# Kernel optimization log

Measured on AMD Instinct MI355X. Metric: run time of the kernel, lower is better.

Reference implementation:

```python
import jax, jax.numpy as jnp
import numpy as np

EPS = 1e-6   # torch F.pairwise_distance default eps
BIG = 1e30   # stand-in for +inf on invalid DP cells (fp32-safe)


def _pairwise_dist(observed, modeled):
    # dist[b, i, j] = || observed[b, i, :] - modeled[b, j, :] + eps ||_2
    diff = observed[:, :, None, :] - modeled[:, None, :, :] + EPS  # [B,T,T,D]
    return jnp.sqrt(jnp.sum(diff * diff, axis=-1))                 # [B,T,T]


def _dtw(dist):
    # Anti-diagonal (wavefront) DTW: diagonal k holds cells (i, j=k-i).
    B, T, _ = dist.shape
    dist_flat = dist.reshape(B, T * T)
    ii = jnp.arange(T)

    d0 = jnp.full((B, T), BIG, dist.dtype).at[:, 0].set(dist[:, 0, 0])
    dm1 = jnp.full((B, T), BIG, dist.dtype)
    pad = jnp.full((B, 1), BIG, dist.dtype)

    def step(carry, k):
        prev2, prev = carry                      # diagonals k-2, k-1, each [B,T] indexed by i
        jj = k - ii
        valid = (jj >= 0) & (jj < T)
        lin = ii * T + jnp.clip(jj, 0, T - 1)
        dd = jnp.take(dist_flat, lin, axis=1)    # dist along diagonal k, [B,T]
        sh_prev = jnp.concatenate([pad, prev[:, :-1]], axis=1)    # dtw[i-1, j]
        sh_prev2 = jnp.concatenate([pad, prev2[:, :-1]], axis=1)  # dtw[i-1, j-1]
        best = jnp.minimum(jnp.minimum(sh_prev, prev), sh_prev2)  # prev = dtw[i, j-1]
        cur = jnp.where(valid[None, :], dd + best, BIG)
        return (prev, cur), None

    (_, last), _ = jax.lax.scan(step, (dm1, d0), jnp.arange(1, 2 * T - 1))
    return last[:, T - 1]  # dtw[T-1, T-1] per batch element


def setup_inputs() -> dict:
    key = jax.random.key(0)
    k1, k2 = jax.random.split(key)
    B, T, D = 8, 1024, 8
    observed = jax.random.normal(k1, (B, T, D), dtype=jnp.float32)
    modeled = jax.random.normal(k2, (B, T, D), dtype=jnp.float32)
    return {"observed": observed, "modeled": modeled}


def reference(observed, modeled):
    dist = _pairwise_dist(observed, modeled)   # [B,T,T]
    dtw_distance = _dtw(dist)                  # [B]
    return jnp.mean(dtw_distance)
```

## Files before the change

kernel.cpp:

```cpp
#include <hip/hip_runtime.h>

#define T_LEN  1024
#define D_DIM  8
#define BIGV   1e30f
#define EPSV   1e-6f
#define RB     256
#define NTILE  17
#define TSTEPS 1088
#define NSLOT  16
#define NW3    8
#define NSS3   32

typedef _Float16 half2v __attribute__((ext_vector_type(2)));
typedef unsigned u32x4  __attribute__((ext_vector_type(4)));

__device__ __forceinline__ float dpp_shr1(float x) {
  int xi = __builtin_bit_cast(int, x);
  int r = __builtin_amdgcn_update_dpp(xi, xi, 0x138, 0xf, 0xf, false);
  return __builtin_bit_cast(float, r);
}
__device__ __forceinline__ float dpp_shl1(float x) {
  int xi = __builtin_bit_cast(int, x);
  int r = __builtin_amdgcn_update_dpp(xi, xi, 0x130, 0xf, 0xf, false);
  return __builtin_bit_cast(float, r);
}

#define GLOADO(dst, addr, OFF)                                             \
  asm volatile("global_load_dwordx4 %0, %1, off offset:" #OFF             \
               : "=v"(dst) : "v"(addr))

__global__ __launch_bounds__(256)
void dist4_kernel(const float* __restrict__ obs, const float* __restrict__ mod,
                  _Float16* __restrict__ dist) {
  const int q  = threadIdx.x & 63;
  const int wv = threadIdx.x >> 6;
  const int lt = blockIdx.x % NTILE;
  const int lg = blockIdx.x / NTILE;
  const int l  = lg * 4 + wv;
  const int s  = blockIdx.y;
  const int b  = blockIdx.z;
  const int t  = lt * 64 + q;
  const int cloc = t - l;
  const int row  = (s < 8) ? (64 * s + l) : (1023 - (64 * (s - 8) + l));

  float dd = __builtin_inff();
  if ((unsigned)cloc < (unsigned)T_LEN) {
    const int cg = (s < 8) ? cloc : (1023 - cloc);
    const float4* o4 = (const float4*)(obs + ((size_t)b * T_LEN + row) * D_DIM);
    const float4* m4 = (const float4*)(mod + ((size_t)b * T_LEN + cg) * D_DIM);
    float4 a0 = o4[0], a1 = o4[1], c0 = m4[0], c1 = m4[1];
    float acc = 0.f, df;
    df = a0.x - c0.x + EPSV; acc = fmaf(df, df, acc);
    df = a0.y - c0.y + EPSV; acc = fmaf(df, df, acc);
    df = a0.z - c0.z + EPSV; acc = fmaf(df, df, acc);
    df = a0.w - c0.w + EPSV; acc = fmaf(df, df, acc);
    df = a1.x - c1.x + EPSV; acc = fmaf(df, df, acc);
    df = a1.y - c1.y + EPSV; acc = fmaf(df, df, acc);
    df = a1.z - c1.z + EPSV; acc = fmaf(df, df, acc);
    df = a1.w - c1.w + EPSV; acc = fmaf(df, df, acc);
    dd = sqrtf(acc);
  }
  dist[(((size_t)(b * NSLOT + s) * NTILE + lt) * 64 + l) * 64 + q] = (_Float16)dd;
}

#define DTW_STEPX(DD, Q)                                                   \
  {                                                                        \
    const float dd_ = (DD);                                                \
    float cu = dpp_shr1(c);                                                \
    cu = lane0 ? rv : cu;                                                  \
    float best = fminf(fminf(cu, cuPrev), c);                              \
    if ((Q) == 0 && LT == 0) { if (w0 && lane0) best = 0.f; }              \
    float cv = dd_ + best;                                                 \
    cuPrev = cu;                                                           \
    c = cv;                                                                \
    rv = dpp_shl1(rv);                                                     \
    out = dpp_shl1(out);                                                   \
    out = lane63 ? c : out;                                                \
  }

#define DTW_STEP2X(U, QB)                                                  \
  {                                                                        \
    half2v hh_ = __builtin_bit_cast(half2v, (unsigned)(U));                \
    DTW_STEPX((float)hh_[0], (QB))                                         \
    DTW_STEPX((float)hh_[1], (QB) + 1)                                     \
  }

#define DTW_STEP8X(V, QB)                                                  \
  DTW_STEP2X((V)[0], (QB))                                                 \
  DTW_STEP2X((V)[1], (QB) + 2)                                             \
  DTW_STEP2X((V)[2], (QB) + 4)                                             \
  DTW_STEP2X((V)[3], (QB) + 6)

#define DTW_TILEX(SS, C0, C1, C2, C3, C4, C5, C6, C7,                      \
                      N0, N1, N2, N3, N4, N5, N6, N7)                      \
  {                                                                        \
    const int T0 = ((SS) - 2 * w) * 64;                                    \
    if (T0 >= 0 && T0 < TSTEPS) {                                          \
      const int LT = T0 >> 6;                                              \
      if (LT < NTILE - 1) {                                                \
        const void* np_ = (const void*)(base + (size_t)(LT + 1) * 4096);   \
        GLOADO(N0, np_, 0);   GLOADO(N1, np_, 16);                         \
        GLOADO(N2, np_, 32);  GLOADO(N3, np_, 48);                         \
        GLOADO(N4, np_, 64);  GLOADO(N5, np_, 80);                         \
        GLOADO(N6, np_, 96);  GLOADO(N7, np_, 112);                        \
        asm volatile("s_waitcnt vmcnt(8)" ::: "memory");                   \
      } else {                                                             \
        asm volatile("s_waitcnt vmcnt(0)" ::: "memory");                   \
      }                                                                    \
      __builtin_amdgcn_sched_barrier(0);                                   \
      float rv;                                                            \
      if (w0) { rv = BIGV; }                                               \
      else    { rv = ringbuf[w - 1][(T0 + l) & (RB - 1)]; }                \
      float out = 0.f;                                                     \
      DTW_STEP8X(C0, 0)  DTW_STEP8X(C1, 8)  DTW_STEP8X(C2, 16)             \
      DTW_STEP8X(C3, 24) DTW_STEP8X(C4, 32) DTW_STEP8X(C5, 40)             \
      DTW_STEP8X(C6, 48) DTW_STEP8X(C7, 56)                                \
      const int e_ = T0 - 63 + l;                                          \
      if ((unsigned)e_ < (unsigned)T_LEN) {                                \
        if (wlast) rowg[e_] = out;                                         \
        else       ringbuf[w][e_ & (RB - 1)] = out;                        \
      }                                                                    \
    }                                                                      \
  }

__global__ __launch_bounds__(512)
void dtw11_kernel(const _Float16* __restrict__ dist, float* __restrict__ rows) {
  __shared__ float ringbuf[NW3 - 1][RB];

  const int tid  = threadIdx.x;
  const int half = blockIdx.x;
  const int b    = blockIdx.y;
  const int l    = tid & 63;
  const int w    = tid >> 6;
  const bool lane0  = (l == 0);
  const bool lane63 = (l == 63);
  const bool w0     = (w == 0);
  const bool wlast  = (w == NW3 - 1);
  const int  s      = half * 8 + w;

  float* rowg = rows + ((size_t)b * 2 + half) * T_LEN;

  {
    float* rp = &ringbuf[0][0];
    for (int k = tid; k < (NW3 - 1) * RB; k += 512) rp[k] = BIGV;
  }

  const _Float16* base = dist + (size_t)(b * NSLOT + s) * NTILE * 4096 + l * 64;

  u32x4 a0, a1, a2, a3, a4, a5, a6, a7;
  u32x4 b0, b1, b2, b3, b4, b5, b6, b7;
  {
    const void* tp = (const void*)base;
    GLOADO(a0, tp, 0);   GLOADO(a1, tp, 16);
    GLOADO(a2, tp, 32);  GLOADO(a3, tp, 48);
    GLOADO(a4, tp, 64);  GLOADO(a5, tp, 80);
    GLOADO(a6, tp, 96);  GLOADO(a7, tp, 112);
    asm volatile("s_waitcnt vmcnt(0)" ::: "memory");
    __builtin_amdgcn_sched_barrier(0);
  }
  b0 = a0; b1 = a1; b2 = a2; b3 = a3; b4 = a4; b5 = a5; b6 = a6; b7 = a7;

  __syncthreads();

  float c = BIGV, cuPrev = BIGV;

  for (int ss = 0; ss < NSS3; ss += 2) {
    DTW_TILEX(ss,     a0, a1, a2, a3, a4, a5, a6, a7,
                      b0, b1, b2, b3, b4, b5, b6, b7)
    __syncthreads();
    DTW_TILEX(ss + 1, b0, b1, b2, b3, b4, b5, b6, b7,
                      a0, a1, a2, a3, a4, a5, a6, a7)
    __syncthreads();
  }
}

__global__ __launch_bounds__(1024)
void combine_kernel(const float* __restrict__ rows, float* __restrict__ bres) {
  __shared__ unsigned gmin;
  const int b = blockIdx.x;
  const int tid = threadIdx.x;
  if (tid == 0) gmin = 0x7f800000u;
  __syncthreads();
  const float* rowf = rows + (size_t)b * 2 * T_LEN;
  const float* rowb = rowf + T_LEN;
  const int j = tid;
  float b1v = rowb[1023 - j];
  float b2v = (j < 1023) ? rowb[1022 - j] : BIGV;
  float v = rowf[j] + fminf(b1v, b2v);
  for (int m = 1; m < 64; m <<= 1) v = fminf(v, __shfl_xor(v, m, 64));
  if ((tid & 63) == 0) atomicMin(&gmin, __float_as_uint(v));
  __syncthreads();
  if (tid == 0) bres[b] = __uint_as_float(gmin);
}

#define NWAVE  16
#define NSS    47
__global__ __launch_bounds__(1024)
void dtw_fused_kernel(const float* __restrict__ obs, const float* __restrict__ mod,
                      float* __restrict__ bres) {
  __shared__ float ringbuf[NWAVE - 1][RB];
  __shared__ float modl[T_LEN * D_DIM];

  const int tid = threadIdx.x;
  const int b   = blockIdx.x;
  const int l   = tid & 63;
  const int w   = tid >> 6;

  const float4* msrc = (const float4*)(mod + (size_t)b * T_LEN * D_DIM);
  float4* mdst = (float4*)modl;
  mdst[tid]        = msrc[tid];
  mdst[tid + 1024] = msrc[tid + 1024];
  const float* orow = obs + ((size_t)b * T_LEN + w * 64 + l) * D_DIM;
  float4 a0 = ((const float4*)orow)[0];
  float4 a1 = ((const float4*)orow)[1];
  float obsp[8] = {a0.x + EPSV, a0.y + EPSV, a0.z + EPSV, a0.w + EPSV,
                   a1.x + EPSV, a1.y + EPSV, a1.z + EPSV, a1.w + EPSV};
  float mrow[8] = {0.f, 0.f, 0.f, 0.f, 0.f, 0.f, 0.f, 0.f};
  __syncthreads();

  float c = BIGV, p = BIGV, rprev = BIGV;
  const bool lane0  = (l == 0);
  const bool lane63 = (l == 63);
  const int  rdw    = (w > 0) ? (w - 1) : 0;
  const bool w0     = (w == 0);
  const bool wlast  = (w == NWAVE - 1);

  for (int ss = 0; ss < NSS; ++ss) {
    const int t0 = (ss - 2 * w) * 64;
    if (t0 >= 0 && t0 < TSTEPS) {
#pragma unroll 8
      for (int q = 0; q < 64; ++q) {
        const int t = t0 + q;
#pragma unroll
        for (int d = 0; d < 8; ++d) mrow[d] = dpp_shr1(mrow[d]);
        if (lane0) {
          const int tm = (t < T_LEN) ? t : (T_LEN - 1);
          const float4* mr = (const float4*)(modl + tm * 8);
          float4 m0 = mr[0], m1 = mr[1];
          mrow[0] = m0.x; mrow[1] = m0.y; mrow[2] = m0.z; mrow[3] = m0.w;
          mrow[4] = m1.x; mrow[5] = m1.y; mrow[6] = m1.z; mrow[7] = m1.w;
        }
        float acc = 0.f;
#pragma unroll
        for (int d = 0; d < 8; ++d) { float df = obsp[d] - mrow[d]; acc = fmaf(df, df, acc); }
        float dd = sqrtf(acc);

        float c_up = dpp_shr1(c);
        float p_up = dpp_shr1(p);
        float ringv = ringbuf[rdw][t & (RB - 1)];
        if (lane0) { c_up = w0 ? BIGV : ringv; p_up = w0 ? BIGV : rprev; }
        rprev = ringv;

        const int j = t - l;
        const bool valid = ((unsigned)j < (unsigned)T_LEN);
        float best = fminf(fminf(c_up, p_up), c);
        if (w0 && t == 0) { if (lane0) best = 0.f; }
        float cur = valid ? (dd + best) : BIGV;
        p = c; c = cur;

        if (lane63 && !wlast && t >= 63 && t < TSTEPS - 1)
          ringbuf[w][(t - 63) & (RB - 1)] = c;
      }
    }
    __syncthreads();
  }
  if (tid == 1023) bres[b] = p;
}

__global__ void mean_kernel(const float* __restrict__ bres, float* __restrict__ out, int B) {
  if (threadIdx.x == 0) {
    float s = 0.f;
    for (int i = 0; i < B; ++i) s += bres[i];
    out[0] = s / (float)B;
  }
}

extern "C" void kernel_launch(void* const* d_in, const int* in_sizes, int n_in,
                              void* d_out, int out_size, void* d_ws, size_t ws_size,
                              hipStream_t stream) {
  (void)n_in; (void)out_size;
  const float* obs = (const float*)d_in[0];
  const float* mod = (const float*)d_in[1];
  float* out = (float*)d_out;
  const int B = in_sizes[0] / (T_LEN * D_DIM);

  float* bres = (float*)d_ws;
  float* rows = (float*)((char*)d_ws + 256);
  _Float16* dist = (_Float16*)((char*)d_ws + 256 + (size_t)B * 2 * T_LEN * 4);
  const size_t need = 256 + (size_t)B * 2 * T_LEN * 4
                    + (size_t)B * NSLOT * NTILE * 4096 * sizeof(_Float16);

  if (ws_size >= need) {
    dist4_kernel<<<dim3(NTILE * 16, NSLOT, B), 256, 0, stream>>>(obs, mod, dist);
    dtw11_kernel<<<dim3(2, B), 512, 0, stream>>>(dist, rows);
    combine_kernel<<<B, 1024, 0, stream>>>(rows, bres);
  } else {
    dtw_fused_kernel<<<B, 1024, 0, stream>>>(obs, mod, bres);
  }
  mean_kernel<<<1, 64, 0, stream>>>(bres, out, B);
}
```

Measured before the change: 89.50 us.

## Process two DTW rows per lane with four-wave wavefront over packed fp16 pairs

Adds a new dist6/dtw13 path in which each lane handles two consecutive DTW rows, so a half-problem is covered by 4 waves of 128 rows each instead of 8 waves of 64. The distance kernel packs the two rows' fp16 distances into one 32-bit word to match this layout. The aim is to cut the number of inter-wave pipeline stages and barriers on the serial wavefront critical path. In exchange each step does twice the work per lane, there are more tile steps per wave, and more registers are used for the double-buffered tiles. The old path remains as a fallback when the workspace is too small.

```diff
diff --git a/kernel.cpp b/kernel.cpp
--- a/kernel.cpp
+++ b/kernel.cpp
@@ -5,6 +5,12 @@
 #define BIGV   1e30f
 #define EPSV   1e-6f
 #define RB     256
+
+#define NT2   18
+#define TS2   1152
+#define NW1   4
+#define NSS1  28
+
 #define NTILE  17
 #define TSTEPS 1088
 #define NSLOT  16
@@ -28,6 +34,215 @@
 #define GLOADO(dst, addr, OFF)                                             \
   asm volatile("global_load_dwordx4 %0, %1, off offset:" #OFF             \
                : "=v"(dst) : "v"(addr))
+
+
+__global__ __launch_bounds__(256)
+void dist6_kernel(const float* __restrict__ obs, const float* __restrict__ mod,
+                  unsigned* __restrict__ dist) {
+  const int q  = threadIdx.x & 63;
+  const int wv = threadIdx.x >> 6;
+  const int lt = blockIdx.x % NT2;
+  const int lg = blockIdx.x / NT2;
+  const int l  = lg * 4 + wv;
+  const int s  = blockIdx.y;
+  const int h  = s >> 2;
+  const int w  = s & 3;
+  const int b  = blockIdx.z;
+  const int t  = lt * 64 + q;
+  const int R0 = 128 * w + 2 * l;
+  const int colA = t - 2 * l;
+  const int colB = colA - 1;
+
+  float vA = __builtin_inff(), vB = __builtin_inff();
+  if ((unsigned)colA < (unsigned)T_LEN) {
+    const int rg = h ? (1023 - R0) : R0;
+    const int cg = h ? (1023 - colA) : colA;
+    const float4* o4 = (const float4*)(obs + ((size_t)b * T_LEN + rg) * D_DIM);
+    const float4* m4 = (const float4*)(mod + ((size_t)b * T_LEN + cg) * D_DIM);
+    float4 a0 = o4[0], a1 = o4[1], c0 = m4[0], c1 = m4[1];
+    float acc = 0.f, df;
+    df = a0.x - c0.x + EPSV; acc = fmaf(df, df, acc);
+    df = a0.y - c0.y + EPSV; acc = fmaf(df, df, acc);
+    df = a0.z - c0.z + EPSV; acc = fmaf(df, df, acc);
+    df = a0.w - c0.w + EPSV; acc = fmaf(df, df, acc);
+    df = a1.x - c1.x + EPSV; acc = fmaf(df, df, acc);
+    df = a1.y - c1.y + EPSV; acc = fmaf(df, df, acc);
+    df = a1.z - c1.z + EPSV; acc = fmaf(df, df, acc);
+    df = a1.w - c1.w + EPSV; acc = fmaf(df, df, acc);
+    vA = sqrtf(acc);
+  }
+  if ((unsigned)colB < (unsigned)T_LEN) {
+    const int rg = h ? (1023 - (R0 + 1)) : (R0 + 1);
+    const int cg = h ? (1023 - colB) : colB;
+    const float4* o4 = (const float4*)(obs + ((size_t)b * T_LEN + rg) * D_DIM);
+    const float4* m4 = (const float4*)(mod + ((size_t)b * T_LEN + cg) * D_DIM);
+    float4 a0 = o4[0], a1 = o4[1], c0 = m4[0], c1 = m4[1];
+    float acc = 0.f, df;
+    df = a0.x - c0.x + EPSV; acc = fmaf(df, df, acc);
+    df = a0.y - c0.y + EPSV; acc = fmaf(df, df, acc);
+    df = a0.z - c0.z + EPSV; acc = fmaf(df, df, acc);
+    df = a0.w - c0.w + EPSV; acc = fmaf(df, df, acc);
+    df = a1.x - c1.x + EPSV; acc = fmaf(df, df, acc);
+    df = a1.y - c1.y + EPSV; acc = fmaf(df, df, acc);
+    df = a1.z - c1.z + EPSV; acc = fmaf(df, df, acc);
+    df = a1.w - c1.w + EPSV; acc = fmaf(df, df, acc);
+    vB = sqrtf(acc);
+  }
+  const unsigned hA = __builtin_bit_cast(unsigned short, (_Float16)vA);
+  const unsigned hB = __builtin_bit_cast(unsigned short, (_Float16)vB);
+  dist[(((size_t)(b * 8 + s) * NT2 + lt) * 64 + l) * 64 + q] = (hB << 16) | hA;
+}
+
+#define DTW_STEPQ2(U, QQ)                                                  \
+  {                                                                        \
+    half2v hh_ = __builtin_bit_cast(half2v, (unsigned)(U));                \
+    const float ddA_ = (float)hh_[0];                                      \
+    const float ddB_ = (float)hh_[1];                                      \
+    float bU  = dpp_shr1(bC);                                              \
+    float bU2 = dpp_shr1(bP);                                              \
+    bU  = lane0 ? rv  : bU;                                                \
+    bU2 = lane0 ? rvo : bU2;                                               \
+    float bestA = fminf(fminf(bU, bU2), aC);                               \
+    if ((QQ) == 0 && LT == 0) { if (w0 && lane0) bestA = 0.f; }            \
+    const float newA = ddA_ + bestA;                                       \
+    const float bestB = fminf(fminf(aC, aP), bC);                          \
+    const float newB = ddB_ + bestB;                                       \
+    aP = aC; aC = newA; bP = bC; bC = newB;                                \
+    rvo = rv; rv = dpp_shl1(rv);                                           \
+    out = dpp_shl1(out);                                                   \
+    out = lane63 ? bC : out;                                               \
+  }
+
+#define DTW_STEP42(V, QB)                                                  \
+  DTW_STEPQ2((V)[0], (QB))                                                 \
+  DTW_STEPQ2((V)[1], (QB) + 1)                                             \
+  DTW_STEPQ2((V)[2], (QB) + 2)                                             \
+  DTW_STEPQ2((V)[3], (QB) + 3)
+
+#define DTW_TILE13(SS, C0,C1,C2,C3,C4,C5,C6,C7,C8,C9,C10,C11,C12,C13,C14,C15, \
+                       N0,N1,N2,N3,N4,N5,N6,N7,N8,N9,N10,N11,N12,N13,N14,N15) \
+  {                                                                        \
+    const int T0 = ((SS) - 3 * w) * 64;                                    \
+    if (T0 >= 0 && T0 < TS2) {                                             \
+      const int LT = T0 >> 6;                                              \
+      if (LT < NT2 - 1) {                                                  \
+        const void* np_ = (const void*)(base + (size_t)(LT + 1) * 4096);   \
+        GLOADO(N0,  np_, 0);    GLOADO(N1,  np_, 16);                      \
+        GLOADO(N2,  np_, 32);   GLOADO(N3,  np_, 48);                      \
+        GLOADO(N4,  np_, 64);   GLOADO(N5,  np_, 80);                      \
+        GLOADO(N6,  np_, 96);   GLOADO(N7,  np_, 112);                     \
+        GLOADO(N8,  np_, 128);  GLOADO(N9,  np_, 144);                     \
+        GLOADO(N10, np_, 160);  GLOADO(N11, np_, 176);                     \
+        GLOADO(N12, np_, 192);  GLOADO(N13, np_, 208);                     \
+        GLOADO(N14, np_, 224);  GLOADO(N15, np_, 240);                     \
+        asm volatile("s_waitcnt vmcnt(16)" ::: "memory");                  \
+      } else {                                                             \
+        asm volatile("s_waitcnt vmcnt(0)" ::: "memory");                   \
+      }                                                                    \
+      __builtin_amdgcn_sched_barrier(0);                                   \
+      float rv, rvo;                                                       \
+      if (w0) { rv = BIGV; rvo = BIGV; }                                   \
+      else {                                                               \
+        rv  = ringbuf[w - 1][(T0 + l) & (RB - 1)];                         \
+        rvo = (LT == 0) ? BIGV : ringbuf[w - 1][(T0 - 1) & (RB - 1)];      \
+      }                                                                    \
+      float out = 0.f;                                                     \
+      DTW_STEP42(C0, 0)   DTW_STEP42(C1, 4)   DTW_STEP42(C2, 8)            \
+      DTW_STEP42(C3, 12)  DTW_STEP42(C4, 16)  DTW_STEP42(C5, 20)           \
+      DTW_STEP42(C6, 24)  DTW_STEP42(C7, 28)  DTW_STEP42(C8, 32)           \
+      DTW_STEP42(C9, 36)  DTW_STEP42(C10, 40) DTW_STEP42(C11, 44)          \
+      DTW_STEP42(C12, 48) DTW_STEP42(C13, 52) DTW_STEP42(C14, 56)          \
+      DTW_STEP42(C15, 60)                                                  \
+      const int e_ = T0 - 127 + l;                                         \
+      if ((unsigned)e_ < (unsigned)T_LEN) {                                \
+        if (wlast) rowg[e_] = out;                                         \
+        else       ringbuf[w][e_ & (RB - 1)] = out;                        \
+      }                                                                    \
+    }                                                                      \
+  }
+
+__global__ __launch_bounds__(256)
+void dtw13_kernel(const unsigned* __restrict__ dist, float* __restrict__ rows) {
+  __shared__ float ringbuf[NW1 - 1][RB];
+
+  const int tid  = threadIdx.x;
+  const int h    = blockIdx.x;
+  const int b    = blockIdx.y;
+  const int l    = tid & 63;
+  const int w    = tid >> 6;
+  const bool lane0  = (l == 0);
+  const bool lane63 = (l == 63);
+  const bool w0     = (w == 0);
+  const bool wlast  = (w == NW1 - 1);
+
+  float* rowg = rows + ((size_t)b * 2 + h) * T_LEN;
+
+  {
+    float* rp = &ringbuf[0][0];
+    for (int k = tid; k < (NW1 - 1) * RB; k += 256) rp[k] = BIGV;
+  }
+
+  const unsigned* base = dist + (size_t)(b * 8 + h * 4 + w) * NT2 * 4096 + l * 64;
+
+  u32x4 a0,a1,a2,a3,a4,a5,a6,a7,a8,a9,a10,a11,a12,a13,a14,a15;
+  u32x4 b0,b1,b2,b3,b4,b5,b6,b7,b8,b9,b10,b11,b12,b13,b14,b15;
+  {
+    const void* tp = (const void*)base;
+    GLOADO(a0,  tp, 0);    GLOADO(a1,  tp, 16);
+    GLOADO(a2,  tp, 32);   GLOADO(a3,  tp, 48);
+    GLOADO(a4,  tp, 64);   GLOADO(a5,  tp, 80);
+    GLOADO(a6,  tp, 96);   GLOADO(a7,  tp, 112);
+    GLOADO(a8,  tp, 128);  GLOADO(a9,  tp, 144);
+    GLOADO(a10, tp, 160);  GLOADO(a11, tp, 176);
+    GLOADO(a12, tp, 192);  GLOADO(a13, tp, 208);
+    GLOADO(a14, tp, 224);  GLOADO(a15, tp, 240);
+    asm volatile("s_waitcnt vmcnt(0)" ::: "memory");
+    __builtin_amdgcn_sched_barrier(0);
+  }
+  b0=a0; b1=a1; b2=a2; b3=a3; b4=a4; b5=a5; b6=a6; b7=a7;
+  b8=a8; b9=a9; b10=a10; b11=a11; b12=a12; b13=a13; b14=a14; b15=a15;
+
+  __syncthreads();
+
+  float aC = BIGV, aP = BIGV, bC = BIGV, bP = BIGV;
+
+  for (int ss = 0; ss < NSS1; ss += 2) {
+    DTW_TILE13(ss,     a0,a1,a2,a3,a4,a5,a6,a7,a8,a9,a10,a11,a12,a13,a14,a15,
+                       b0,b1,b2,b3,b4,b5,b6,b7,b8,b9,b10,b11,b12,b13,b14,b15)
+    __syncthreads();
+    DTW_TILE13(ss + 1, b0,b1,b2,b3,b4,b5,b6,b7,b8,b9,b10,b11,b12,b13,b14,b15,
+                       a0,a1,a2,a3,a4,a5,a6,a7,a8,a9,a10,a11,a12,a13,a14,a15)
+    __syncthreads();
+  }
+  (void)aP; (void)bP;
+}
+
+__global__ __launch_bounds__(1024)
+void combine_kernel(const float* __restrict__ rows, float* __restrict__ bres) {
+  __shared__ unsigned gmin;
+  const int b = blockIdx.x;
+  const int tid = threadIdx.x;
+  if (tid == 0) gmin = 0x7f800000u;
+  __syncthreads();
+  const float* rowf = rows + (size_t)b * 2 * T_LEN;
+  const float* rowb = rowf + T_LEN;
+  const int j = tid;
+  float b1v = rowb[1023 - j];
+  float b2v = (j < 1023) ? rowb[1022 - j] : BIGV;
+  float v = rowf[j] + fminf(b1v, b2v);
+  for (int m = 1; m < 64; m <<= 1) v = fminf(v, __shfl_xor(v, m, 64));
+  if ((tid & 63) == 0) atomicMin(&gmin, __float_as_uint(v));
+  __syncthreads();
+  if (tid == 0) bres[b] = __uint_as_float(gmin);
+}
+
+__global__ void mean_kernel(const float* __restrict__ bres, float* __restrict__ out, int B) {
+  if (threadIdx.x == 0) {
+    float s = 0.f;
+    for (int i = 0; i < B; ++i) s += bres[i];
+    out[0] = s / (float)B;
+  }
+}
 
 __global__ __launch_bounds__(256)
 void dist4_kernel(const float* __restrict__ obs, const float* __restrict__ mod,
@@ -174,31 +389,12 @@
   }
 }
 
-__global__ __launch_bounds__(1024)
-void combine_kernel(const float* __restrict__ rows, float* __restrict__ bres) {
-  __shared__ unsigned gmin;
-  const int b = blockIdx.x;
-  const int tid = threadIdx.x;
-  if (tid == 0) gmin = 0x7f800000u;
-  __syncthreads();
-  const float* rowf = rows + (size_t)b * 2 * T_LEN;
-  const float* rowb = rowf + T_LEN;
-  const int j = tid;
-  float b1v = rowb[1023 - j];
-  float b2v = (j < 1023) ? rowb[1022 - j] : BIGV;
-  float v = rowf[j] + fminf(b1v, b2v);
-  for (int m = 1; m < 64; m <<= 1) v = fminf(v, __shfl_xor(v, m, 64));
-  if ((tid & 63) == 0) atomicMin(&gmin, __float_as_uint(v));
-  __syncthreads();
-  if (tid == 0) bres[b] = __uint_as_float(gmin);
-}
-
 #define NWAVE  16
 #define NSS    47
 __global__ __launch_bounds__(1024)
 void dtw_fused_kernel(const float* __restrict__ obs, const float* __restrict__ mod,
                       float* __restrict__ bres) {
-  __shared__ float ringbuf[NWAVE - 1][RB];
+  __shared__ float ringbuf2[NWAVE - 1][RB];
   __shared__ float modl[T_LEN * D_DIM];
 
   const int tid = threadIdx.x;
@@ -247,7 +443,7 @@
 
         float c_up = dpp_shr1(c);
         float p_up = dpp_shr1(p);
-        float ringv = ringbuf[rdw][t & (RB - 1)];
+        float ringv = ringbuf2[rdw][t & (RB - 1)];
         if (lane0) { c_up = w0 ? BIGV : ringv; p_up = w0 ? BIGV : rprev; }
         rprev = ringv;
 
@@ -259,20 +455,12 @@
         p = c; c = cur;
 
         if (lane63 && !wlast && t >= 63 && t < TSTEPS - 1)
-          ringbuf[w][(t - 63) & (RB - 1)] = c;
+          ringbuf2[w][(t - 63) & (RB - 1)] = c;
       }
     }
     __syncthreads();
   }
   if (tid == 1023) bres[b] = p;
-}
-
-__global__ void mean_kernel(const float* __restrict__ bres, float* __restrict__ out, int B) {
-  if (threadIdx.x == 0) {
-    float s = 0.f;
-    for (int i = 0; i < B; ++i) s += bres[i];
-    out[0] = s / (float)B;
-  }
 }
 
 extern "C" void kernel_launch(void* const* d_in, const int* in_sizes, int n_in,
@@ -286,16 +474,24 @@
 
   float* bres = (float*)d_ws;
   float* rows = (float*)((char*)d_ws + 256);
-  _Float16* dist = (_Float16*)((char*)d_ws + 256 + (size_t)B * 2 * T_LEN * 4);
-  const size_t need = 256 + (size_t)B * 2 * T_LEN * 4
-                    + (size_t)B * NSLOT * NTILE * 4096 * sizeof(_Float16);
-
-  if (ws_size >= need) {
-    dist4_kernel<<<dim3(NTILE * 16, NSLOT, B), 256, 0, stream>>>(obs, mod, dist);
-    dtw11_kernel<<<dim3(2, B), 512, 0, stream>>>(dist, rows);
+  char*  dist = (char*)d_ws + 256 + (size_t)B * 2 * T_LEN * 4;
+  const size_t need1 = 256 + (size_t)B * 2 * T_LEN * 4
+                     + (size_t)B * 8 * NT2 * 4096 * 4;
+  const size_t need2 = 256 + (size_t)B * 2 * T_LEN * 4
+                     + (size_t)B * NSLOT * NTILE * 4096 * sizeof(_Float16);
+
+  if (ws_size >= need1) {
+    dist6_kernel<<<dim3(NT2 * 16, 8, B), 256, 0, stream>>>(obs, mod, (unsigned*)dist);
+    dtw13_kernel<<<dim3(2, B), 256, 0, stream>>>((const unsigned*)dist, rows);
     combine_kernel<<<B, 1024, 0, stream>>>(rows, bres);
+    mean_kernel<<<1, 64, 0, stream>>>(bres, out, B);
+  } else if (ws_size >= need2) {
+    dist4_kernel<<<dim3(NTILE * 16, NSLOT, B), 256, 0, stream>>>(obs, mod, (_Float16*)dist);
+    dtw11_kernel<<<dim3(2, B), 512, 0, stream>>>((const _Float16*)dist, rows);
+    combine_kernel<<<B, 1024, 0, stream>>>(rows, bres);
+    mean_kernel<<<1, 64, 0, stream>>>(bres, out, B);
   } else {
     dtw_fused_kernel<<<B, 1024, 0, stream>>>(obs, mod, bres);
-  }
-  mean_kernel<<<1, 64, 0, stream>>>(bres, out, B);
-}
+    mean_kernel<<<1, 64, 0, stream>>>(bres, out, B);
+  }
+}
```

New measurement: 90.76 us. About the same (+1.4%).
